# Kernel optimization log

Measured on AMD Instinct MI355X. Metric: run time of the kernel, lower is better.

The kernel has to match this reference:

```python
import jax, jax.numpy as jnp
import numpy as np

D_MODEL = 1024
N_HEADS = 16
D_KEY = D_MODEL // N_HEADS
NEG = -1e9


def setup_inputs() -> dict:
    key = jax.random.key(0)
    ks = jax.random.split(key, 10)
    B, S = 4, 2048
    s = 0.02
    query = jax.random.normal(ks[0], (B, S, D_MODEL), dtype=jnp.float32)
    # causal mask: 1 where attend allowed, 0 where masked (masked_fill(mask==0, -1e9))
    mask = jnp.tril(jnp.ones((S, S), dtype=jnp.int32))[None, None]
    Wq = jax.random.normal(ks[1], (D_MODEL, D_MODEL), dtype=jnp.float32) * s
    bq = jax.random.normal(ks[2], (D_MODEL,), dtype=jnp.float32) * s
    Wk = jax.random.normal(ks[3], (D_MODEL, D_MODEL), dtype=jnp.float32) * s
    bk = jax.random.normal(ks[4], (D_MODEL,), dtype=jnp.float32) * s
    Wv = jax.random.normal(ks[5], (D_MODEL, D_MODEL), dtype=jnp.float32) * s
    bv = jax.random.normal(ks[6], (D_MODEL,), dtype=jnp.float32) * s
    Wo = jax.random.normal(ks[7], (D_MODEL, D_MODEL), dtype=jnp.float32) * s
    bo = jax.random.normal(ks[8], (D_MODEL,), dtype=jnp.float32) * s
    return {"query": query, "mask": mask, "Wq": Wq, "bq": bq, "Wk": Wk,
            "bk": bk, "Wv": Wv, "bv": bv, "Wo": Wo, "bo": bo}


def _split_heads(x):
    B, S, _ = x.shape
    return x.reshape(B, S, N_HEADS, D_KEY).transpose(0, 2, 1, 3)  # [B,H,S,Dk]


def reference(query, mask, Wq, bq, Wk, bk, Wv, bv, Wo, bo):
    B, S, _ = query.shape
    # torch Linear: x @ W^T + b
    q = _split_heads(query @ Wq.T + bq)
    k = _split_heads(query @ Wk.T + bk)  # self-attention: key_value is None
    v = _split_heads(query @ Wv.T + bv)
    scores = jnp.einsum('bhqd,bhkd->bhqk', q, k) / jnp.sqrt(jnp.float32(D_KEY))
    scores = jnp.where(mask == 0, jnp.float32(NEG), scores)
    weights = jax.nn.softmax(scores, axis=-1)  # dropout=0 (eval)
    attn = jnp.einsum('bhqk,bhkd->bhqd', weights, v)
    merged = attn.transpose(0, 2, 1, 3).reshape(B, S, D_MODEL)
    return merged @ Wo.T + bo
```

## Files before the change

kernel.cpp:

```cpp
#include <hip/hip_runtime.h>
#include <hip/hip_bf16.h>

typedef __attribute__((ext_vector_type(8))) short bf16x8;
typedef __attribute__((ext_vector_type(4))) float f32x4;
typedef __attribute__((ext_vector_type(16))) float f32x16;
typedef __attribute__((ext_vector_type(2))) unsigned int u32x2;

__device__ __forceinline__ float fexp2(float x) { return __builtin_amdgcn_exp2f(x); }

__device__ __forceinline__ ushort f2bf(float x) {
    union { float f; unsigned u; } c; c.f = x;
    unsigned r = c.u + 0x7fff + ((c.u >> 16) & 1);
    return (ushort)(r >> 16);
}

__device__ __forceinline__ unsigned cvtpk(float lo, float hi) {
    unsigned r;
    asm("v_cvt_pk_bf16_f32 %0, %1, %2" : "=v"(r) : "v"(lo), "v"(hi));
    return r;
}

__device__ __forceinline__ void gload16(const void* g, void* l) {
    __builtin_amdgcn_global_load_lds((const __attribute__((address_space(1))) void*)g,
                                     (__attribute__((address_space(3))) void*)l, 16, 0, 0);
}

__device__ __forceinline__ void blockbar() {
    asm volatile("" ::: "memory");
    __builtin_amdgcn_s_barrier();
    asm volatile("" ::: "memory");
}

__global__ void cvt_f32_bf16(const float* __restrict__ in, ushort* __restrict__ out, int n4) {
    int i = blockIdx.x * blockDim.x + threadIdx.x;
    int stride = gridDim.x * blockDim.x;
    for (; i < n4; i += stride) {
        float4 v = ((const float4*)in)[i];
        ushort4 o;
        o.x = f2bf(v.x); o.y = f2bf(v.y); o.z = f2bf(v.z); o.w = f2bf(v.w);
        ((ushort4*)out)[i] = o;
    }
}

__global__ void cvt_w4(const float* __restrict__ a, const float* __restrict__ b,
                       const float* __restrict__ c, const float* __restrict__ d,
                       ushort* __restrict__ oq, ushort* __restrict__ ow) {
    const int N4 = 262144;
    int i = blockIdx.x * blockDim.x + threadIdx.x;
    int stride = gridDim.x * blockDim.x;
    for (; i < 4 * N4; i += stride) {
        int sel = i >> 18, local = i & (N4 - 1);
        const float* src = (sel == 0) ? a : (sel == 1) ? b : (sel == 2) ? c : d;
        float4 v = ((const float4*)src)[local];
        ushort4 o;
        o.x = f2bf(v.x); o.y = f2bf(v.y); o.z = f2bf(v.z); o.w = f2bf(v.w);
        if (sel < 3) ((ushort4*)oq)[sel * N4 + local] = o;
        else         ((ushort4*)ow)[local] = o;
    }
}

template<int MODE>
__global__ __launch_bounds__(512, 2)
void gemm_p2(const ushort* __restrict__ A, const ushort* __restrict__ Bt,
             const float* __restrict__ bias0, const float* __restrict__ bias1,
             const float* __restrict__ bias2,
             ushort* __restrict__ outb, float* __restrict__ outf,
             int M, int N, int K) {
    __shared__ ushort lds[49152];
    const int t = threadIdx.x, lane = t & 63, w = t >> 6;
    const int wm = w >> 1, wn = w & 1;
    const int l15 = lane & 15, lg = lane >> 4;
    const int sw7 = l15 & 7;

    const int nbx = N >> 7;
    const int nwg = nbx * (M >> 8);
    const int bid = blockIdx.y * nbx + blockIdx.x;
    const int swz = (bid & 7) * (nwg >> 3) + (bid >> 3);
    const int m0 = (swz / nbx) * 256, n0 = (swz % nbx) * 128;

    const int srow = lane >> 3;
    const int gcb = (lane & 7) ^ srow;
    const ushort* gsrc[6];
#pragma unroll
    for (int s = 0; s < 4; s++)
        gsrc[s] = A + (size_t)(m0 + s * 64 + w * 8 + srow) * K + gcb * 8;
#pragma unroll
    for (int s = 0; s < 2; s++)
        gsrc[4 + s] = Bt + (size_t)(n0 + s * 64 + w * 8 + srow) * K + gcb * 8;

#define STAGE(ST, KT) { \
    ushort* dst = &lds[(ST) * 24576 + w * 512]; \
    gload16(gsrc[0] + (KT) * 64, dst); \
    gload16(gsrc[1] + (KT) * 64, dst + 4096); \
    gload16(gsrc[2] + (KT) * 64, dst + 8192); \
    gload16(gsrc[3] + (KT) * 64, dst + 12288); \
    gload16(gsrc[4] + (KT) * 64, dst + 16384); \
    gload16(gsrc[5] + (KT) * 64, dst + 20480); }

    f32x4 acc[4][4] = {};
    const int NT = K >> 6;

    STAGE(0, 0); STAGE(1, 1);

    for (int kt = 0; kt < NT; ++kt) {
        if (kt < NT - 1) asm volatile("s_waitcnt vmcnt(6)" ::: "memory");
        else             asm volatile("s_waitcnt vmcnt(0)" ::: "memory");
        blockbar();

        const ushort* stg = &lds[(kt & 1) * 24576];
        bf16x8 a0[4], b0[4], a1[4], b1[4];
#pragma unroll
        for (int mi = 0; mi < 4; mi++) {
            int row = wm * 64 + mi * 16 + l15;
            a0[mi] = *(const bf16x8*)&stg[row * 64 + ((lg ^ sw7) << 3)];
            a1[mi] = *(const bf16x8*)&stg[row * 64 + (((4 + lg) ^ sw7) << 3)];
        }
#pragma unroll
        for (int ni = 0; ni < 4; ni++) {
            int row = wn * 64 + ni * 16 + l15;
            b0[ni] = *(const bf16x8*)&stg[16384 + row * 64 + ((lg ^ sw7) << 3)];
            b1[ni] = *(const bf16x8*)&stg[16384 + row * 64 + (((4 + lg) ^ sw7) << 3)];
        }

        __builtin_amdgcn_s_setprio(1);
#pragma unroll
        for (int mi = 0; mi < 4; mi++)
#pragma unroll
            for (int ni = 0; ni < 4; ni++)
                acc[mi][ni] = __builtin_amdgcn_mfma_f32_16x16x32_bf16(a0[mi], b0[ni], acc[mi][ni], 0, 0, 0);
        __builtin_amdgcn_s_setprio(0);

        asm volatile("s_waitcnt lgkmcnt(0)" ::: "memory");
        blockbar();
        if (kt + 2 < NT) STAGE((kt & 1), kt + 2);

        __builtin_amdgcn_s_setprio(1);
#pragma unroll
        for (int mi = 0; mi < 4; mi++)
#pragma unroll
            for (int ni = 0; ni < 4; ni++)
                acc[mi][ni] = __builtin_amdgcn_mfma_f32_16x16x32_bf16(a1[mi], b1[ni], acc[mi][ni], 0, 0, 0);
        __builtin_amdgcn_s_setprio(0);
    }
#undef STAGE

#pragma unroll
    for (int mi = 0; mi < 4; mi++)
#pragma unroll
        for (int ni = 0; ni < 4; ni++)
#pragma unroll
            for (int r = 0; r < 4; r++) {
                int gm = m0 + wm * 64 + mi * 16 + lg * 4 + r;
                int gn = n0 + wn * 64 + ni * 16 + l15;
                if (MODE == 0) {
                    const float* bp = (gn < 1024) ? bias0 : ((gn < 2048) ? bias1 : bias2);
                    float v = acc[mi][ni][r] + bp[gn & 1023];
                    if (gn < 1024) v *= 0.18033688011f;
                    int proj = gn >> 10, nn = gn & 1023;
                    int h = nn >> 6, d = nn & 63;
                    int b = gm >> 11, s = gm & 2047;
                    outb[(size_t)proj * 8388608 + ((((size_t)b << 4) + h) * 2048 + s) * 64 + d] = f2bf(v);
                } else {
                    outf[(size_t)gm * N + gn] = acc[mi][ni][r] + bias0[gn];
                }
            }
}

__global__ __launch_bounds__(256, 3)
void attn_fwd(const ushort* __restrict__ Qb, const ushort* __restrict__ Kb,
              const ushort* __restrict__ Vb, ushort* __restrict__ Ab) {
    constexpr int S = 2048;
    __shared__ ushort lds[16384];

    const int bid = blockIdx.x;
    const int qt = 15 - (bid >> 6);
    const int bh = bid & 63;
    const int b = bh >> 4, h = bh & 15;
    const ushort* Qp = Qb + (size_t)bh * S * 64;
    const ushort* Kp = Kb + (size_t)bh * S * 64;
    const ushort* Vp = Vb + (size_t)bh * S * 64;

    const int t = threadIdx.x, lane = t & 63, w = t >> 6;
    const int l15 = lane & 15, l31 = lane & 31, hi = lane >> 5, g = lane >> 4;

    int koff[2], voff[2];
#pragma unroll
    for (int i = 0; i < 2; i++) {
        int row = (w * 2 + i) * 8 + (lane >> 3);
        int gg = (lane & 7) ^ ((row ^ (row >> 3)) & 7);
        koff[i] = row * 64 + gg * 8;
    }
#pragma unroll
    for (int it = 0; it < 2; it++) {
        int T = (it * 4 + w) * 64 + lane;
        int kvb = T >> 5, db = (T >> 3) & 3, kvr = (T >> 1) & 3, dh = T & 1;
        voff[it] = (kvb * 4 + kvr) * 64 + db * 16 + dh * 8;
    }
    const unsigned vtbase = (unsigned)(uintptr_t)&lds[8192]
                          + (hi << 10) + ((g & 1) << 7) + (l15 << 3);

    auto stage = [&](int phase, int k0) {
#pragma unroll
        for (int i = 0; i < 2; i++)
            gload16(Kp + (size_t)k0 * 64 + koff[i], &lds[(phase << 12) + ((w * 2 + i) << 9)]);
#pragma unroll
        for (int it = 0; it < 2; it++)
            gload16(Vp + (size_t)k0 * 64 + voff[it], &lds[8192 + (phase << 12) + (((it << 2) + w) << 9)]);
    };

    const int fb = qt * 128 + w * 32;
    const int nt = 2 * qt + 2;

    bf16x8 qf[4];
#pragma unroll
    for (int kc = 0; kc < 4; kc++)
        qf[kc] = *(const bf16x8*)&Qp[(size_t)(fb + l31) * 64 + kc * 16 + hi * 8];

    float m = -3e38f, ls = 0.f;
    f32x16 O0 = {}, O1 = {};

    stage(0, 0);

    for (int tile = 0; tile < nt; tile++) {
        const int phase = tile & 1;
        const int k0 = tile * 64;
        if (tile + 1 < nt) {
            stage(phase ^ 1, (tile + 1) * 64);
            asm volatile("s_waitcnt vmcnt(4)" ::: "memory");
        } else {
            asm volatile("s_waitcnt vmcnt(0)" ::: "memory");
        }
        blockbar();

        if (k0 <= fb + 31) {
            const ushort* Kc = &lds[phase << 12];
            f32x16 s0 = {}, s1 = {};
            {
                bf16x8 kf[4];
#pragma unroll
                for (int kc = 0; kc < 4; kc++) {
                    int row = l31;
                    int sw = (row ^ (row >> 3)) & 7;
                    kf[kc] = *(const bf16x8*)&Kc[row * 64 + (((kc * 2 + hi) ^ sw) << 3)];
                }
                __builtin_amdgcn_s_setprio(1);
#pragma unroll
                for (int kc = 0; kc < 4; kc++)
                    s0 = __builtin_amdgcn_mfma_f32_32x32x16_bf16(kf[kc], qf[kc], s0, 0, 0, 0);
                __builtin_amdgcn_s_setprio(0);
            }
            {
                bf16x8 kf[4];
#pragma unroll
                for (int kc = 0; kc < 4; kc++) {
                    int row = 32 + l31;
                    int sw = (row ^ (row >> 3)) & 7;
                    kf[kc] = *(const bf16x8*)&Kc[row * 64 + (((kc * 2 + hi) ^ sw) << 3)];
                }
                __builtin_amdgcn_s_setprio(1);
#pragma unroll
                for (int kc = 0; kc < 4; kc++)
                    s1 = __builtin_amdgcn_mfma_f32_32x32x16_bf16(kf[kc], qf[kc], s1, 0, 0, 0);
                __builtin_amdgcn_s_setprio(0);
            }

            float pv[32];
            const bool diag = (k0 + 63 > fb);
            const int rel = fb + l31 - k0 - 4 * hi;
#pragma unroll
            for (int r = 0; r < 16; r++) {
                float v0 = s0[r], v1 = s1[r];
                if (diag) {
                    int kvc = (r & 3) + 8 * (r >> 2);
                    if (kvc > rel)      v0 = -1e30f;
                    if (kvc + 32 > rel) v1 = -1e30f;
                }
                pv[r] = v0; pv[16 + r] = v1;
            }
            float mx[16];
#pragma unroll
            for (int i = 0; i < 16; i++) mx[i] = fmaxf(pv[i], pv[i + 16]);
#pragma unroll
            for (int sgap = 8; sgap >= 1; sgap >>= 1)
#pragma unroll
                for (int i = 0; i < sgap; i++) mx[i] = fmaxf(mx[i], mx[i + sgap]);
            float pmax = fmaxf(mx[0], __shfl_xor(mx[0], 32));

            if (!__all(pmax <= m + 8.f)) {
                float mnew = fmaxf(m, pmax);
                float a = fexp2(m - mnew);
                ls *= a;
                float ar[16];
#pragma unroll
                for (int r = 0; r < 16; r++)
                    ar[r] = __shfl(a, (r & 3) + 8 * (r >> 2) + 4 * hi, 32);
#pragma unroll
                for (int r = 0; r < 16; r++) { O0[r] *= ar[r]; O1[r] *= ar[r]; }
                m = mnew;
            }
#pragma unroll
            for (int i = 0; i < 32; i++) pv[i] = fexp2(pv[i] - m);
            float sm[16];
#pragma unroll
            for (int i = 0; i < 16; i++) sm[i] = pv[i] + pv[i + 16];
#pragma unroll
            for (int sgap = 8; sgap >= 1; sgap >>= 1)
#pragma unroll
                for (int i = 0; i < sgap; i++) sm[i] += sm[i + sgap];
            ls += sm[0] + __shfl_xor(sm[0], 32);

            union PAu { bf16x8 v; unsigned wd[4]; } PA[4];
#pragma unroll
            for (int ks = 0; ks < 4; ks++)
#pragma unroll
                for (int i = 0; i < 2; i++) {
                    unsigned xw = cvtpk(pv[8 * ks + 2 * i], pv[8 * ks + 2 * i + 1]);
                    unsigned yw = cvtpk(pv[8 * ks + 2 * i + 4], pv[8 * ks + 2 * i + 5]);
                    asm("v_permlane32_swap_b32 %0, %1" : "+v"(xw), "+v"(yw));
                    PA[ks].wd[i] = xw; PA[ks].wd[2 + i] = yw;
                }

            const unsigned vtb = vtbase + (phase << 13);
            u32x2 vb[16];
#define TRR(idx, OFFSTR) asm volatile("ds_read_b64_tr_b16 %0, %1 offset:" OFFSTR : "=v"(vb[idx]) : "v"(vtb))
            TRR(0, "0");    TRR(1, "512");  TRR(2, "2048"); TRR(3, "2560");
            TRR(4, "4096"); TRR(5, "4608"); TRR(6, "6144"); TRR(7, "6656");
            TRR(8, "256");  TRR(9, "768");  TRR(10, "2304"); TRR(11, "2816");
            TRR(12, "4352"); TRR(13, "4864"); TRR(14, "6400"); TRR(15, "6912");
#undef TRR
            union FragU { bf16x8 v; u32x2 hh[2]; };
            asm volatile("s_waitcnt lgkmcnt(8)" ::: "memory");
            __builtin_amdgcn_sched_barrier(0);
            __builtin_amdgcn_s_setprio(1);
#pragma unroll
            for (int ks = 0; ks < 4; ks++) {
                FragU f; f.hh[0] = vb[ks * 2]; f.hh[1] = vb[ks * 2 + 1];
                O0 = __builtin_amdgcn_mfma_f32_32x32x16_bf16(PA[ks].v, f.v, O0, 0, 0, 0);
            }
            __builtin_amdgcn_s_setprio(0);
            asm volatile("s_waitcnt lgkmcnt(0)" ::: "memory");
            __builtin_amdgcn_sched_barrier(0);
            __builtin_amdgcn_s_setprio(1);
#pragma unroll
            for (int ks = 0; ks < 4; ks++) {
                FragU f; f.hh[0] = vb[8 + ks * 2]; f.hh[1] = vb[8 + ks * 2 + 1];
                O1 = __builtin_amdgcn_mfma_f32_32x32x16_bf16(PA[ks].v, f.v, O1, 0, 0, 0);
            }
            __builtin_amdgcn_s_setprio(0);
        }
        blockbar();
    }

    float inv[16];
#pragma unroll
    for (int r = 0; r < 16; r++)
        inv[r] = __builtin_amdgcn_rcpf(__shfl(ls, (r & 3) + 8 * (r >> 2) + 4 * hi, 32));
#pragma unroll
    for (int r = 0; r < 16; r++) {
        int q = fb + (r & 3) + 8 * (r >> 2) + 4 * hi;
        size_t base = ((size_t)b * 2048 + q) * 1024 + h * 64;
        Ab[base + l31]      = f2bf(O0[r] * inv[r]);
        Ab[base + 32 + l31] = f2bf(O1[r] * inv[r]);
    }
}

extern "C" void kernel_launch(void* const* d_in, const int* in_sizes, int n_in,
                              void* d_out, int out_size, void* d_ws, size_t ws_size,
                              hipStream_t stream) {
    const float* query = (const float*)d_in[0];
    const float* Wq = (const float*)d_in[2];
    const float* bq = (const float*)d_in[3];
    const float* Wk = (const float*)d_in[4];
    const float* bk = (const float*)d_in[5];
    const float* Wv = (const float*)d_in[6];
    const float* bv = (const float*)d_in[7];
    const float* Wo = (const float*)d_in[8];
    const float* bo = (const float*)d_in[9];
    float* out = (float*)d_out;

    char* ws = (char*)d_ws;
    const size_t SZ_X = 8192ull * 1024 * 2;
    const size_t SZ_W = 1024ull * 1024 * 2;
    ushort* Xb   = (ushort*)(ws);
    ushort* Wcat = (ushort*)(ws + SZ_X);
    ushort* Wob  = (ushort*)(ws + SZ_X + 3 * SZ_W);
    ushort* QKVb = (ushort*)(ws + SZ_X + 4 * SZ_W);
    ushort* Ab   = (ushort*)(ws + 4 * SZ_X + 4 * SZ_W);

    cvt_f32_bf16<<<1024, 256, 0, stream>>>(query, Xb, 8192 * 1024 / 4);
    cvt_w4<<<1024, 256, 0, stream>>>(Wq, Wk, Wv, Wo, Wcat, Wob);

    gemm_p2<0><<<dim3(3072 / 128, 8192 / 256), 512, 0, stream>>>(
        Xb, Wcat, bq, bk, bv, QKVb, nullptr, 8192, 3072, 1024);

    attn_fwd<<<1024, 256, 0, stream>>>(QKVb, QKVb + 8388608, QKVb + 2 * 8388608, Ab);

    gemm_p2<1><<<dim3(1024 / 128, 8192 / 256), 512, 0, stream>>>(
        Ab, Wob, bo, nullptr, nullptr, nullptr, out, 8192, 1024, 1024);
}
```

Measured before the change: 164.8 us.

## Triple-buffer GEMM LDS stages and interleave half-prefetches with split MFMA phases

The projection GEMM moves from double- to triple-buffered LDS staging, so the prefetch of tile kt+2 goes to a buffer nobody is reading. Each k-iteration is now split into four MFMA phases, with LDS fragment reads spread between them and the global prefetch issued in two halves. Explicit barriers and sched_barriers make the waves issue memory and MFMA work in lockstep. The cost is a 144 KB LDS footprint per block, which likely allows only one 512-thread block per CU instead of two, plus many more block barriers per iteration.

```diff
diff --git a/kernel.cpp b/kernel.cpp
--- a/kernel.cpp
+++ b/kernel.cpp
@@ -61,12 +61,12 @@
 
 template<int MODE>
 __global__ __launch_bounds__(512, 2)
-void gemm_p2(const ushort* __restrict__ A, const ushort* __restrict__ Bt,
+void gemm_p8(const ushort* __restrict__ A, const ushort* __restrict__ Bt,
              const float* __restrict__ bias0, const float* __restrict__ bias1,
              const float* __restrict__ bias2,
              ushort* __restrict__ outb, float* __restrict__ outf,
              int M, int N, int K) {
-    __shared__ ushort lds[49152];
+    __shared__ ushort lds[73728];
     const int t = threadIdx.x, lane = t & 63, w = t >> 6;
     const int wm = w >> 1, wn = w & 1;
     const int l15 = lane & 15, lg = lane >> 4;
@@ -96,6 +96,19 @@
     gload16(gsrc[3] + (KT) * 64, dst + 12288); \
     gload16(gsrc[4] + (KT) * 64, dst + 16384); \
     gload16(gsrc[5] + (KT) * 64, dst + 20480); }
+#define STAGE_H1(ST, KT) { \
+    ushort* dst = &lds[(ST) * 24576 + w * 512]; \
+    gload16(gsrc[0] + (KT) * 64, dst); \
+    gload16(gsrc[1] + (KT) * 64, dst + 4096); \
+    gload16(gsrc[2] + (KT) * 64, dst + 8192); }
+#define STAGE_H2(ST, KT) { \
+    ushort* dst = &lds[(ST) * 24576 + w * 512]; \
+    gload16(gsrc[3] + (KT) * 64, dst + 12288); \
+    gload16(gsrc[4] + (KT) * 64, dst + 16384); \
+    gload16(gsrc[5] + (KT) * 64, dst + 20480); }
+
+#define RDA(stg, mi, kb) (*(const bf16x8*)&(stg)[(wm * 64 + (mi) * 16 + l15) * 64 + ((((kb) + lg) ^ sw7) << 3)])
+#define RDB(stg, ni, kb) (*(const bf16x8*)&(stg)[16384 + (wn * 64 + (ni) * 16 + l15) * 64 + ((((kb) + lg) ^ sw7) << 3)])
 
     f32x4 acc[4][4] = {};
     const int NT = K >> 6;
@@ -107,42 +120,73 @@
         else             asm volatile("s_waitcnt vmcnt(0)" ::: "memory");
         blockbar();
 
-        const ushort* stg = &lds[(kt & 1) * 24576];
+        const ushort* stg = &lds[(kt % 3) * 24576];
+        const int st2 = (kt + 2) % 3;
+        const bool pf = (kt + 2 < NT);
         bf16x8 a0[4], b0[4], a1[4], b1[4];
-#pragma unroll
-        for (int mi = 0; mi < 4; mi++) {
-            int row = wm * 64 + mi * 16 + l15;
-            a0[mi] = *(const bf16x8*)&stg[row * 64 + ((lg ^ sw7) << 3)];
-            a1[mi] = *(const bf16x8*)&stg[row * 64 + (((4 + lg) ^ sw7) << 3)];
-        }
-#pragma unroll
-        for (int ni = 0; ni < 4; ni++) {
-            int row = wn * 64 + ni * 16 + l15;
-            b0[ni] = *(const bf16x8*)&stg[16384 + row * 64 + ((lg ^ sw7) << 3)];
-            b1[ni] = *(const bf16x8*)&stg[16384 + row * 64 + (((4 + lg) ^ sw7) << 3)];
-        }
-
+
+        a0[0] = RDA(stg, 0, 0); a0[1] = RDA(stg, 1, 0);
+        b0[0] = RDB(stg, 0, 0); b0[1] = RDB(stg, 1, 0);
+        b0[2] = RDB(stg, 2, 0); b0[3] = RDB(stg, 3, 0);
+        if (pf) STAGE_H1(st2, kt + 2);
+        blockbar();
+        asm volatile("s_waitcnt lgkmcnt(0)" ::: "memory");
+        __builtin_amdgcn_sched_barrier(0);
         __builtin_amdgcn_s_setprio(1);
 #pragma unroll
-        for (int mi = 0; mi < 4; mi++)
+        for (int mi = 0; mi < 2; mi++)
 #pragma unroll
             for (int ni = 0; ni < 4; ni++)
                 acc[mi][ni] = __builtin_amdgcn_mfma_f32_16x16x32_bf16(a0[mi], b0[ni], acc[mi][ni], 0, 0, 0);
         __builtin_amdgcn_s_setprio(0);
-
+        blockbar();
+
+        a0[2] = RDA(stg, 2, 0); a0[3] = RDA(stg, 3, 0);
+        if (pf) STAGE_H2(st2, kt + 2);
+        blockbar();
         asm volatile("s_waitcnt lgkmcnt(0)" ::: "memory");
-        blockbar();
-        if (kt + 2 < NT) STAGE((kt & 1), kt + 2);
-
+        __builtin_amdgcn_sched_barrier(0);
         __builtin_amdgcn_s_setprio(1);
 #pragma unroll
-        for (int mi = 0; mi < 4; mi++)
+        for (int mi = 2; mi < 4; mi++)
+#pragma unroll
+            for (int ni = 0; ni < 4; ni++)
+                acc[mi][ni] = __builtin_amdgcn_mfma_f32_16x16x32_bf16(a0[mi], b0[ni], acc[mi][ni], 0, 0, 0);
+        __builtin_amdgcn_s_setprio(0);
+        blockbar();
+
+        a1[0] = RDA(stg, 0, 4); a1[1] = RDA(stg, 1, 4);
+        b1[0] = RDB(stg, 0, 4); b1[1] = RDB(stg, 1, 4);
+        b1[2] = RDB(stg, 2, 4); b1[3] = RDB(stg, 3, 4);
+        blockbar();
+        asm volatile("s_waitcnt lgkmcnt(0)" ::: "memory");
+        __builtin_amdgcn_sched_barrier(0);
+        __builtin_amdgcn_s_setprio(1);
+#pragma unroll
+        for (int mi = 0; mi < 2; mi++)
 #pragma unroll
             for (int ni = 0; ni < 4; ni++)
                 acc[mi][ni] = __builtin_amdgcn_mfma_f32_16x16x32_bf16(a1[mi], b1[ni], acc[mi][ni], 0, 0, 0);
         __builtin_amdgcn_s_setprio(0);
+        blockbar();
+
+        a1[2] = RDA(stg, 2, 4); a1[3] = RDA(stg, 3, 4);
+        blockbar();
+        asm volatile("s_waitcnt lgkmcnt(0)" ::: "memory");
+        __builtin_amdgcn_sched_barrier(0);
+        __builtin_amdgcn_s_setprio(1);
+#pragma unroll
+        for (int mi = 2; mi < 4; mi++)
+#pragma unroll
+            for (int ni = 0; ni < 4; ni++)
+                acc[mi][ni] = __builtin_amdgcn_mfma_f32_16x16x32_bf16(a1[mi], b1[ni], acc[mi][ni], 0, 0, 0);
+        __builtin_amdgcn_s_setprio(0);
     }
 #undef STAGE
+#undef STAGE_H1
+#undef STAGE_H2
+#undef RDA
+#undef RDB
 
 #pragma unroll
     for (int mi = 0; mi < 4; mi++)
@@ -390,11 +434,11 @@
     cvt_f32_bf16<<<1024, 256, 0, stream>>>(query, Xb, 8192 * 1024 / 4);
     cvt_w4<<<1024, 256, 0, stream>>>(Wq, Wk, Wv, Wo, Wcat, Wob);
 
-    gemm_p2<0><<<dim3(3072 / 128, 8192 / 256), 512, 0, stream>>>(
+    gemm_p8<0><<<dim3(3072 / 128, 8192 / 256), 512, 0, stream>>>(
         Xb, Wcat, bq, bk, bv, QKVb, nullptr, 8192, 3072, 1024);
 
     attn_fwd<<<1024, 256, 0, stream>>>(QKVb, QKVb + 8388608, QKVb + 2 * 8388608, Ab);
 
-    gemm_p2<1><<<dim3(1024 / 128, 8192 / 256), 512, 0, stream>>>(
+    gemm_p8<1><<<dim3(1024 / 128, 8192 / 256), 512, 0, stream>>>(
         Ab, Wob, bo, nullptr, nullptr, nullptr, out, 8192, 1024, 1024);
 }
```

After: 168.3 us. +2.1%, slower.
